# Optimization experiments

Measured on AMD Instinct MI355X. Metric: run time of the kernel, lower is better.

The kernel has to match this reference:

```python
import jax, jax.numpy as jnp
import numpy as np

ALPHA = 0.2       # LeakyReLU negative slope
OUT_FEATURES = 256
NEG_INF = -9e15   # matches -9000000000000000.0 in the torch code

N = 8192
IN_FEATURES = 512


def setup_inputs() -> dict:
    key = jax.random.key(0)
    k1, k2, k3, k4 = jax.random.split(key, 4)
    h = jax.random.normal(k1, (N, IN_FEATURES), dtype=jnp.float32)
    adj = jax.random.randint(k2, (N, N), 0, 2, dtype=jnp.int32)
    # xavier-uniform-like init scales (exact init values don't matter for correctness)
    W = jax.random.normal(k3, (IN_FEATURES, OUT_FEATURES), dtype=jnp.float32) * 0.05
    a = jax.random.normal(k4, (2 * OUT_FEATURES, 1), dtype=jnp.float32) * 0.05
    return {"h": h, "adj": adj, "W": W, "a": a, "split_name": 0}


def reference(h, adj, W, a, split_name):
    # h: [N, Fin], W: [Fin, Fout], a: [2*Fout, 1], adj: [N, N]
    Wh = h @ W                                   # [N, Fout]
    Wh1 = Wh @ a[:OUT_FEATURES, :]               # [N, 1]
    Wh2 = Wh @ a[OUT_FEATURES:, :]               # [N, 1]
    e = jax.nn.leaky_relu(Wh1 + Wh2.T, negative_slope=ALPHA)  # [N, N]
    mask = adj > 0
    scores = jnp.where(mask, e, jnp.float32(NEG_INF))
    attention = jax.nn.softmax(scores, axis=1)
    # dropout is identity in eval mode (training=False)
    attention = jnp.where(mask, attention, jnp.float32(0.0))
    h_prime = attention @ Wh                     # [N, Fout]
    return jax.nn.elu(h_prime)                   # concat=True -> elu
```

## Files before the change

kernel.cpp:

```cpp
#include <hip/hip_runtime.h>

#define NN 8192
#define FIN 512
#define FOUT 256
#define JS 8
#define STRIP 1024
#define NSTEP 32

typedef _Float16 f16;
typedef __attribute__((ext_vector_type(8))) _Float16 f16x8;
typedef __attribute__((ext_vector_type(4))) _Float16 f16x4;
typedef __attribute__((ext_vector_type(4))) float f32x4;
typedef __attribute__((ext_vector_type(16))) float f32x16;
typedef __attribute__((ext_vector_type(4))) int i32x4;
typedef unsigned long long u64;

__device__ __forceinline__ float lrelu(float x) { return fmaxf(x, 0.2f * x); }

__global__ void k_cvtprep(const int* __restrict__ adj, u64* __restrict__ maskG,
                          const float* __restrict__ W, f16* __restrict__ wth,
                          f16* __restrict__ wtl) {
  int bid = blockIdx.x;
  int tid = threadIdx.x;
  if (bid < NN / 4) {
    int gw = bid * 4 + (tid >> 6);
    int l = tid & 63;
    const int* src = adj + (size_t)gw * NN + 4 * l;
    u64* dst = maskG + (size_t)gw * 128;
    i32x4 v[4];
#pragma unroll
    for (int p = 0; p < 4; ++p)
      v[p] = __builtin_nontemporal_load((const i32x4*)(src + p * 256));
#pragma unroll 1
    for (int p = 0; p < 32; ++p) {
      i32x4 cur = v[p & 3];
      u64 b0 = __ballot(cur[0] > 0);
      u64 b1 = __ballot(cur[1] > 0);
      u64 b2 = __ballot(cur[2] > 0);
      u64 b3 = __ballot(cur[3] > 0);
      if (p + 4 < 32)
        v[p & 3] = __builtin_nontemporal_load((const i32x4*)(src + (p + 4) * 256));
      if (l < 4) {
        u64 bb = (l == 0) ? b0 : (l == 1) ? b1 : (l == 2) ? b2 : b3;
        dst[p * 4 + l] = bb;
      }
    }
  } else {
    int id = (bid - NN / 4) * 256 + tid;
    int c = id >> 9, k = id & 511;
    float v = W[k * FOUT + c];
    f16 a = (f16)v;
    wth[c * FIN + k] = a;
    wtl[c * FIN + k] = (f16)(v - (float)a);
  }
}

__launch_bounds__(256, 2)
__global__ void k_gemm1(const float* __restrict__ h, const f16* __restrict__ wth,
                        const f16* __restrict__ wtl, const float* __restrict__ avec,
                        f16* __restrict__ whT16, float* __restrict__ wh1,
                        float* __restrict__ wh2) {
  int i0 = blockIdx.x * 32;
  int tid = threadIdx.x;
  int w = tid >> 6, l = tid & 63, m = l & 15, g = l >> 4;
  f32x4 acc[2][4] = {};
#pragma unroll 1
  for (int k0 = 0; k0 < FIN; k0 += 32) {
    f16x8 ah[2], al[2], bh[4], bl[4];
#pragma unroll
    for (int rf = 0; rf < 2; ++rf) {
      int ro = (i0 + 16 * rf + m) * FIN + k0 + 8 * g;
      f32x4 va = *(const f32x4*)(h + ro);
      f32x4 vb = *(const f32x4*)(h + ro + 4);
#pragma unroll
      for (int e = 0; e < 4; ++e) {
        f16 x = (f16)va[e];
        ah[rf][e] = x;
        al[rf][e] = (f16)(va[e] - (float)x);
        f16 y = (f16)vb[e];
        ah[rf][4 + e] = y;
        al[rf][4 + e] = (f16)(vb[e] - (float)y);
      }
    }
#pragma unroll
    for (int cf = 0; cf < 4; ++cf) {
      int co = (64 * w + 16 * cf + m) * FIN + k0 + 8 * g;
      bh[cf] = *(const f16x8*)(wth + co);
      bl[cf] = *(const f16x8*)(wtl + co);
    }
#pragma unroll
    for (int rf = 0; rf < 2; ++rf)
#pragma unroll
      for (int cf = 0; cf < 4; ++cf) {
        acc[rf][cf] = __builtin_amdgcn_mfma_f32_16x16x32_f16(ah[rf], bh[cf], acc[rf][cf], 0, 0, 0);
        acc[rf][cf] = __builtin_amdgcn_mfma_f32_16x16x32_f16(ah[rf], bl[cf], acc[rf][cf], 0, 0, 0);
        acc[rf][cf] = __builtin_amdgcn_mfma_f32_16x16x32_f16(al[rf], bh[cf], acc[rf][cf], 0, 0, 0);
      }
  }
  __shared__ float tile[32][FOUT + 1];
#pragma unroll
  for (int rf = 0; rf < 2; ++rf)
#pragma unroll
    for (int cf = 0; cf < 4; ++cf)
#pragma unroll
      for (int r = 0; r < 4; ++r)
        tile[16 * rf + 4 * g + r][64 * w + 16 * cf + m] = acc[rf][cf][r];
  __syncthreads();
  {
    int c = tid;
    f16x8 vv[4];
#pragma unroll
    for (int r = 0; r < 32; ++r) vv[r >> 3][r & 7] = (f16)tile[r][c];
    size_t base = ((size_t)(i0 >> 4) * 256 + c) * 16;
    *(f16x8*)(whT16 + base) = vv[0];
    *(f16x8*)(whT16 + base + 8) = vv[1];
    *(f16x8*)(whT16 + base + 4096) = vv[2];
    *(f16x8*)(whT16 + base + 4096 + 8) = vv[3];
  }
  {
    int r = tid >> 3, ls = tid & 7;
    float s1 = 0.f, s2 = 0.f;
    for (int c = ls; c < FOUT; c += 8) {
      float v = tile[r][c];
      s1 = fmaf(v, avec[c], s1);
      s2 = fmaf(v, avec[FOUT + c], s2);
    }
#pragma unroll
    for (int off = 1; off < 8; off <<= 1) {
      s1 += __shfl_xor(s1, off);
      s2 += __shfl_xor(s2, off);
    }
    if (ls == 0) {
      wh1[i0 + r] = s1;
      wh2[i0 + r] = s2;
    }
  }
}

__global__ void k_maxprep(const float* __restrict__ wh1, const float* __restrict__ wh2,
                          float* __restrict__ e1p, float* __restrict__ e1n,
                          float* __restrict__ thr, float* __restrict__ e2p,
                          float* __restrict__ e2n) {
  int t = threadIdx.x;
  float mx = -1e30f;
  for (int i = t; i < NN; i += 256) mx = fmaxf(mx, wh2[i]);
#pragma unroll
  for (int off = 1; off < 64; off <<= 1) mx = fmaxf(mx, __shfl_xor(mx, off));
  __shared__ float sm[4];
  if ((t & 63) == 0) sm[t >> 6] = mx;
  __syncthreads();
  float M2 = fmaxf(fmaxf(sm[0], sm[1]), fmaxf(sm[2], sm[3]));
  const float L = 1.4426950408889634f;
  int i = blockIdx.x * 256 + t;
  float w1 = wh1[i], w2 = wh2[i];
  float m = lrelu(w1 + M2);
  e1p[i] = exp2f((w1 - m) * L);
  e1n[i] = exp2f((0.2f * w1 - m) * L);
  thr[i] = exp2f(-w1 * L);
  e2p[i] = exp2f(w2 * L);
  e2n[i] = exp2f(0.2f * w2 * L);
}

__launch_bounds__(256, 2)
__global__ void k_attn(const u64* __restrict__ maskG, const f16* __restrict__ whT16,
                       const float* __restrict__ e1pA, const float* __restrict__ e1nA,
                       const float* __restrict__ thrA, const float* __restrict__ e2pA,
                       const float* __restrict__ e2nA, f16* __restrict__ accP,
                       float* __restrict__ zP) {
  int bx = blockIdx.x;
  int js = bx & (JS - 1), rb = bx >> 3;
  int i0b = rb * 128;
  int jbase = js * STRIP;
  int tid = threadIdx.x, w = tid >> 6, l = tid & 63;
  int lr = l & 31, hi = l >> 5;
  int row = i0b + w * 32 + lr;

  __shared__ u64 mrow[4][32][18];
  __shared__ __align__(16) char ldsB[2][16384];

#pragma unroll
  for (int p = 0; p < 4; ++p) {
    int r = 8 * p + (l >> 3);
    const i32x4* src =
        (const i32x4*)(maskG + (size_t)(i0b + 32 * w + r) * 128 + js * 16) + (l & 7);
    *(i32x4*)(&mrow[w][r][(l & 7) * 2]) = *src;
  }

  float E1p = e1pA[row], E1n = e1nA[row], T = thrA[row];
  f32x16 acc[8] = {};
  float za = 0.f;

  const size_t jb16 = (size_t)(jbase >> 4) * 4096;
  const float* e2pb = e2pA + jbase + 8 * hi;
  const float* e2nb = e2nA + jbase + 8 * hi;

  int ldst[4];
  size_t gsrc[4];
#pragma unroll
  for (int r = 0; r < 4; ++r) {
    int g = r * 256 + tid;
    gsrc[r] = (size_t)(g >> 9) * 4096 + 8 * (g & 511);
    ldst[r] = (g >> 9) * 8192 + ((16 * (g & 511)) ^ (((g >> 3) & 7) << 4));
  }
  int rdbase = (lr * 32 + hi * 16) ^ (((lr >> 2) & 7) << 4);

  i32x4 stg[4];
#pragma unroll
  for (int r = 0; r < 4; ++r)
    stg[r] = __builtin_nontemporal_load((const i32x4*)(whT16 + jb16 + gsrc[r]));
#pragma unroll
  for (int r = 0; r < 4; ++r) *(i32x4*)(&ldsB[0][ldst[r]]) = stg[r];
  __syncthreads();

#pragma unroll 1
  for (int ch = 0; ch < 4; ++ch) {
    u64 wr0[4];
#pragma unroll
    for (int q = 0; q < 4; ++q) wr0[q] = mrow[w][lr][ch * 4 + q];
#pragma unroll 1
    for (int ts = 0; ts < 8; ++ts) {
      int t = ch * 8 + ts;
      int cur = t & 1;
      int jc = t * 32;
      if (t + 1 < NSTEP) {
        const f16* src = whT16 + jb16 + (size_t)(2 * (t + 1)) * 4096;
#pragma unroll
        for (int r = 0; r < 4; ++r)
          stg[r] = __builtin_nontemporal_load((const i32x4*)(src + gsrc[r]));
      }
      int sb = ts * 8 + 2 * hi;
      unsigned b4[4];
#pragma unroll
      for (int e = 0; e < 4; ++e) b4[e] = (unsigned)(wr0[e] >> sb);
      f16x8 pa0, pa1;
#pragma unroll
      for (int q = 0; q < 2; ++q) {
        int fo = jc + 4 * q;
        f32x4 ep0 = *(const f32x4*)(e2pb + fo);
        f32x4 en0 = *(const f32x4*)(e2nb + fo);
        f32x4 ep1 = *(const f32x4*)(e2pb + fo + 16);
        f32x4 en1 = *(const f32x4*)(e2nb + fo + 16);
#pragma unroll
        for (int e = 0; e < 4; ++e) {
          int f = 4 * q + e;
          bool s0 = ep0[e] >= T;
          float v0 = (s0 ? E1p : E1n) * (s0 ? ep0[e] : en0[e]);
          v0 = ((b4[e] >> q) & 1u) ? v0 : 0.f;
          za += v0;
          pa0[f] = (f16)v0;
          bool s1 = ep1[e] >= T;
          float v1 = (s1 ? E1p : E1n) * (s1 ? ep1[e] : en1[e]);
          v1 = ((b4[e] >> (4 + q)) & 1u) ? v1 : 0.f;
          za += v1;
          pa1[f] = (f16)v1;
        }
      }
#pragma unroll
      for (int cf = 0; cf < 8; ++cf) {
        f16x8 bf0 = *(const f16x8*)(&ldsB[cur][cf * 1024 + rdbase]);
        acc[cf] = __builtin_amdgcn_mfma_f32_32x32x16_f16(pa0, bf0, acc[cf], 0, 0, 0);
      }
#pragma unroll
      for (int cf = 0; cf < 8; ++cf) {
        f16x8 bf1 = *(const f16x8*)(&ldsB[cur][8192 + cf * 1024 + rdbase]);
        acc[cf] = __builtin_amdgcn_mfma_f32_32x32x16_f16(pa1, bf1, acc[cf], 0, 0, 0);
      }
      if (t + 1 < NSTEP) {
#pragma unroll
        for (int r = 0; r < 4; ++r) *(i32x4*)(&ldsB[cur ^ 1][ldst[r]]) = stg[r];
        __syncthreads();
      }
    }
  }

  za += __shfl_xor(za, 32);
  if (hi == 0) zP[(size_t)js * NN + row] = za;

  f16* ap = accP + (size_t)js * NN * FOUT;
#pragma unroll
  for (int c = 0; c < 8; ++c)
#pragma unroll
    for (int r = 0; r < 16; ++r) {
      int grow = i0b + 32 * w + (r & 3) + 8 * (r >> 2) + 4 * hi;
      int gcol = c * 32 + lr;
      __builtin_nontemporal_store((f16)acc[c][r], ap + (size_t)grow * FOUT + gcol);
    }
}

__global__ void k_combine(const f16* __restrict__ accP, const float* __restrict__ zP,
                          float* __restrict__ out) {
  int id = blockIdx.x * 256 + threadIdx.x;
  size_t idx = (size_t)id * 8;
  int row = (int)(idx >> 8);
  float s[8] = {};
#pragma unroll
  for (int p = 0; p < JS; ++p) {
    f16x8 v = *(const f16x8*)(accP + (size_t)p * NN * FOUT + idx);
#pragma unroll
    for (int i = 0; i < 8; ++i) s[i] += (float)v[i];
  }
  float z = 0.f;
#pragma unroll
  for (int p = 0; p < JS; ++p) z += zP[(size_t)p * NN + row];
  float inv = (z > 0.f) ? 1.f / z : 0.f;
  f32x4 o0, o1;
#pragma unroll
  for (int i = 0; i < 4; ++i) {
    float x0 = s[i] * inv;
    o0[i] = (x0 > 0.f) ? x0 : expm1f(x0);
    float x1 = s[4 + i] * inv;
    o1[i] = (x1 > 0.f) ? x1 : expm1f(x1);
  }
  *(f32x4*)(out + idx) = o0;
  *(f32x4*)(out + idx + 4) = o1;
}

extern "C" void kernel_launch(void* const* d_in, const int* in_sizes, int n_in,
                              void* d_out, int out_size, void* d_ws, size_t ws_size,
                              hipStream_t stream) {
  const float* h = (const float*)d_in[0];
  const int* adj = (const int*)d_in[1];
  const float* W = (const float*)d_in[2];
  const float* a = (const float*)d_in[3];
  (void)in_sizes; (void)n_in; (void)out_size; (void)ws_size;

  char* ws = (char*)d_ws;
  size_t off = 0;
  auto alloc = [&](size_t bytes) {
    void* p = ws + off;
    off = (off + bytes + 255) & ~(size_t)255;
    return p;
  };
  f16* accP = (f16*)alloc((size_t)JS * NN * FOUT * 2);
  u64* maskG = (u64*)alloc((size_t)NN * 128 * 8);
  f16* whT16 = (f16*)alloc((size_t)FOUT * NN * 2);
  f16* wth = (f16*)alloc((size_t)FOUT * FIN * 2);
  f16* wtl = (f16*)alloc((size_t)FOUT * FIN * 2);
  float* wh1 = (float*)alloc((size_t)NN * 4);
  float* wh2 = (float*)alloc((size_t)NN * 4);
  float* e1p = (float*)alloc((size_t)NN * 4);
  float* e1n = (float*)alloc((size_t)NN * 4);
  float* thr = (float*)alloc((size_t)NN * 4);
  float* e2p = (float*)alloc((size_t)NN * 4);
  float* e2n = (float*)alloc((size_t)NN * 4);
  float* zP = (float*)alloc((size_t)JS * NN * 4);

  k_cvtprep<<<NN / 4 + FIN * FOUT / 256, 256, 0, stream>>>(adj, maskG, W, wth, wtl);
  k_gemm1<<<NN / 32, 256, 0, stream>>>(h, wth, wtl, a, whT16, wh1, wh2);
  k_maxprep<<<NN / 256, 256, 0, stream>>>(wh1, wh2, e1p, e1n, thr, e2p, e2n);
  k_attn<<<(NN / 128) * JS, 256, 0, stream>>>(maskG, whT16, e1p, e1n, thr, e2p, e2n,
                                              accP, zP);
  k_combine<<<NN * FOUT / 2048, 256, 0, stream>>>(accP, zP, (float*)d_out);
}
```

Measured before the change: 152.9 us.

## Switch attention kernel to 16x16x32 MFMA with 64-row blocks

Reworks the attention-aggregation kernel from 32x32x16 MFMA tiles on 128-row blocks to 16x16x32 MFMA tiles on 64-row blocks. Each wave now covers 16 rows with one f16x8 A operand per step instead of two, and uses 16 f32x4 accumulators instead of 8 f32x16. The grid doubles, and launch bounds are raised to 3 blocks per SM to improve occupancy. In exchange, each Wh tile staged in LDS is reused by half as many rows, so global and LDS traffic per output grows.

```diff
diff --git a/kernel.cpp b/kernel.cpp
--- a/kernel.cpp
+++ b/kernel.cpp
@@ -161,7 +161,7 @@
   e2n[i] = exp2f(0.2f * w2 * L);
 }
 
-__launch_bounds__(256, 2)
+__launch_bounds__(256, 3)
 __global__ void k_attn(const u64* __restrict__ maskG, const f16* __restrict__ whT16,
                        const float* __restrict__ e1pA, const float* __restrict__ e1nA,
                        const float* __restrict__ thrA, const float* __restrict__ e2pA,
@@ -169,40 +169,41 @@
                        float* __restrict__ zP) {
   int bx = blockIdx.x;
   int js = bx & (JS - 1), rb = bx >> 3;
-  int i0b = rb * 128;
+  int i0b = rb * 64;
   int jbase = js * STRIP;
   int tid = threadIdx.x, w = tid >> 6, l = tid & 63;
-  int lr = l & 31, hi = l >> 5;
-  int row = i0b + w * 32 + lr;
-
-  __shared__ u64 mrow[4][32][18];
+  int m = l & 15, g = l >> 4;
+  int row = i0b + w * 16 + m;
+
+  __shared__ u64 mrow[4][16][18];
   __shared__ __align__(16) char ldsB[2][16384];
 
-#pragma unroll
-  for (int p = 0; p < 4; ++p) {
-    int r = 8 * p + (l >> 3);
+  {
+    int r = l >> 2, wd = (l & 3) * 4;
     const i32x4* src =
-        (const i32x4*)(maskG + (size_t)(i0b + 32 * w + r) * 128 + js * 16) + (l & 7);
-    *(i32x4*)(&mrow[w][r][(l & 7) * 2]) = *src;
+        (const i32x4*)(maskG + (size_t)(i0b + w * 16 + r) * 128 + js * 16 + wd);
+    *(i32x4*)(&mrow[w][r][wd]) = src[0];
+    *(i32x4*)(&mrow[w][r][wd + 2]) = src[1];
   }
 
   float E1p = e1pA[row], E1n = e1nA[row], T = thrA[row];
-  f32x16 acc[8] = {};
+  f32x4 acc[16] = {};
   float za = 0.f;
 
   const size_t jb16 = (size_t)(jbase >> 4) * 4096;
-  const float* e2pb = e2pA + jbase + 8 * hi;
-  const float* e2nb = e2nA + jbase + 8 * hi;
+  const float* e2pb = e2pA + jbase + 8 * g;
+  const float* e2nb = e2nA + jbase + 8 * g;
 
   int ldst[4];
   size_t gsrc[4];
 #pragma unroll
   for (int r = 0; r < 4; ++r) {
-    int g = r * 256 + tid;
-    gsrc[r] = (size_t)(g >> 9) * 4096 + 8 * (g & 511);
-    ldst[r] = (g >> 9) * 8192 + ((16 * (g & 511)) ^ (((g >> 3) & 7) << 4));
-  }
-  int rdbase = (lr * 32 + hi * 16) ^ (((lr >> 2) & 7) << 4);
+    int gg = r * 256 + tid;
+    gsrc[r] = (size_t)(gg >> 9) * 4096 + 8 * (gg & 511);
+    ldst[r] = (gg >> 9) * 8192 + ((16 * (gg & 511)) ^ (((gg >> 3) & 7) << 4));
+  }
+  int kbb = (g >> 1) * 8192;
+  int n0 = 2 * m + (g & 1);
 
   i32x4 stg[4];
 #pragma unroll
@@ -216,7 +217,7 @@
   for (int ch = 0; ch < 4; ++ch) {
     u64 wr0[4];
 #pragma unroll
-    for (int q = 0; q < 4; ++q) wr0[q] = mrow[w][lr][ch * 4 + q];
+    for (int q = 0; q < 4; ++q) wr0[q] = mrow[w][m][ch * 4 + q];
 #pragma unroll 1
     for (int ts = 0; ts < 8; ++ts) {
       int t = ch * 8 + ts;
@@ -228,42 +229,40 @@
         for (int r = 0; r < 4; ++r)
           stg[r] = __builtin_nontemporal_load((const i32x4*)(src + gsrc[r]));
       }
-      int sb = ts * 8 + 2 * hi;
+      int sb = ts * 8 + 2 * g;
       unsigned b4[4];
 #pragma unroll
       for (int e = 0; e < 4; ++e) b4[e] = (unsigned)(wr0[e] >> sb);
-      f16x8 pa0, pa1;
-#pragma unroll
-      for (int q = 0; q < 2; ++q) {
-        int fo = jc + 4 * q;
-        f32x4 ep0 = *(const f32x4*)(e2pb + fo);
-        f32x4 en0 = *(const f32x4*)(e2nb + fo);
-        f32x4 ep1 = *(const f32x4*)(e2pb + fo + 16);
-        f32x4 en1 = *(const f32x4*)(e2nb + fo + 16);
-#pragma unroll
-        for (int e = 0; e < 4; ++e) {
-          int f = 4 * q + e;
-          bool s0 = ep0[e] >= T;
-          float v0 = (s0 ? E1p : E1n) * (s0 ? ep0[e] : en0[e]);
-          v0 = ((b4[e] >> q) & 1u) ? v0 : 0.f;
-          za += v0;
-          pa0[f] = (f16)v0;
-          bool s1 = ep1[e] >= T;
-          float v1 = (s1 ? E1p : E1n) * (s1 ? ep1[e] : en1[e]);
-          v1 = ((b4[e] >> (4 + q)) & 1u) ? v1 : 0.f;
-          za += v1;
-          pa1[f] = (f16)v1;
+      f32x4 ep0 = *(const f32x4*)(e2pb + jc);
+      f32x4 en0 = *(const f32x4*)(e2nb + jc);
+      f32x4 ep1 = *(const f32x4*)(e2pb + jc + 4);
+      f32x4 en1 = *(const f32x4*)(e2nb + jc + 4);
+      f16x8 pa;
+#pragma unroll
+      for (int e = 0; e < 4; ++e) {
+        bool s0 = ep0[e] >= T;
+        float v0 = (s0 ? E1p : E1n) * (s0 ? ep0[e] : en0[e]);
+        v0 = (b4[e] & 1u) ? v0 : 0.f;
+        za += v0;
+        pa[e] = (f16)v0;
+        bool s1 = ep1[e] >= T;
+        float v1 = (s1 ? E1p : E1n) * (s1 ? ep1[e] : en1[e]);
+        v1 = ((b4[e] >> 1) & 1u) ? v1 : 0.f;
+        za += v1;
+        pa[4 + e] = (f16)v1;
+      }
+#pragma unroll
+      for (int cg = 0; cg < 4; ++cg) {
+        f16x8 bf[4];
+#pragma unroll
+        for (int c = 0; c < 4; ++c) {
+          int n = n0 + 32 * (4 * cg + c);
+          bf[c] = *(const f16x8*)(&ldsB[cur][kbb + ((16 * n) ^ (((n >> 3) & 7) << 4))]);
         }
-      }
-#pragma unroll
-      for (int cf = 0; cf < 8; ++cf) {
-        f16x8 bf0 = *(const f16x8*)(&ldsB[cur][cf * 1024 + rdbase]);
-        acc[cf] = __builtin_amdgcn_mfma_f32_32x32x16_f16(pa0, bf0, acc[cf], 0, 0, 0);
-      }
-#pragma unroll
-      for (int cf = 0; cf < 8; ++cf) {
-        f16x8 bf1 = *(const f16x8*)(&ldsB[cur][8192 + cf * 1024 + rdbase]);
-        acc[cf] = __builtin_amdgcn_mfma_f32_32x32x16_f16(pa1, bf1, acc[cf], 0, 0, 0);
+#pragma unroll
+        for (int c = 0; c < 4; ++c)
+          acc[4 * cg + c] =
+              __builtin_amdgcn_mfma_f32_16x16x32_f16(pa, bf[c], acc[4 * cg + c], 0, 0, 0);
       }
       if (t + 1 < NSTEP) {
 #pragma unroll
@@ -273,17 +272,18 @@
     }
   }
 
+  za += __shfl_xor(za, 16);
   za += __shfl_xor(za, 32);
-  if (hi == 0) zP[(size_t)js * NN + row] = za;
+  if (l < 16) zP[(size_t)js * NN + i0b + w * 16 + m] = za;
 
   f16* ap = accP + (size_t)js * NN * FOUT;
 #pragma unroll
-  for (int c = 0; c < 8; ++c)
-#pragma unroll
-    for (int r = 0; r < 16; ++r) {
-      int grow = i0b + 32 * w + (r & 3) + 8 * (r >> 2) + 4 * hi;
-      int gcol = c * 32 + lr;
-      __builtin_nontemporal_store((f16)acc[c][r], ap + (size_t)grow * FOUT + gcol);
+  for (int cf = 0; cf < 16; ++cf)
+#pragma unroll
+    for (int r = 0; r < 4; ++r) {
+      int grow = i0b + w * 16 + 4 * g + r;
+      int gcol = cf * 16 + m;
+      __builtin_nontemporal_store((f16)acc[cf][r], ap + (size_t)grow * FOUT + gcol);
     }
 }
 
@@ -348,7 +348,7 @@
   k_cvtprep<<<NN / 4 + FIN * FOUT / 256, 256, 0, stream>>>(adj, maskG, W, wth, wtl);
   k_gemm1<<<NN / 32, 256, 0, stream>>>(h, wth, wtl, a, whT16, wh1, wh2);
   k_maxprep<<<NN / 256, 256, 0, stream>>>(wh1, wh2, e1p, e1n, thr, e2p, e2n);
-  k_attn<<<(NN / 128) * JS, 256, 0, stream>>>(maskG, whT16, e1p, e1n, thr, e2p, e2n,
-                                              accP, zP);
+  k_attn<<<(NN / 64) * JS, 256, 0, stream>>>(maskG, whT16, e1p, e1n, thr, e2p, e2n,
+                                             accP, zP);
   k_combine<<<NN * FOUT / 2048, 256, 0, stream>>>(accP, zP, (float*)d_out);
 }
```

New measurement: 189.5 us. 24.0% more time.
